# Performance work log

Measured on AMD Instinct MI355X. Metric: run time of the kernel, lower is better.

The kernel has to match this reference:

```python
import jax, jax.numpy as jnp
import numpy as np

N_INPUTS = 128
N_LATENT = 21
LEN_TIME = 51
NUM_SHIFTS = 50
BATCH = 2048
N_HIDDEN = 4  # hidden relu layers in the outer DenseResBlock


def setup_inputs() -> dict:
    key = jax.random.key(0)
    ks = jax.random.split(key, 8)
    s = 0.05  # small init scale keeps activations sane through the residual stack
    return {
        "inputs": jax.random.normal(ks[0], (BATCH, LEN_TIME, N_INPUTS), jnp.float32),
        "L": jnp.eye(N_LATENT, dtype=jnp.float32)
             + s * jax.random.normal(ks[1], (N_LATENT, N_LATENT), jnp.float32),
        "ienc_W": s * jax.random.normal(ks[2], (N_INPUTS, N_LATENT), jnp.float32),
        "idec_W": s * jax.random.normal(ks[3], (N_LATENT, N_INPUTS), jnp.float32),
        "enc_W": s * jax.random.normal(ks[4], (N_HIDDEN, N_INPUTS, N_INPUTS), jnp.float32),
        "enc_b": jnp.zeros((N_HIDDEN, N_INPUTS), jnp.float32),
        "enc_Wo": s * jax.random.normal(ks[5], (N_INPUTS, N_INPUTS), jnp.float32),
        "enc_bo": jnp.zeros((N_INPUTS,), jnp.float32),
        "dec_W": s * jax.random.normal(ks[6], (N_HIDDEN, N_INPUTS, N_INPUTS), jnp.float32),
        "dec_b": jnp.zeros((N_HIDDEN, N_INPUTS), jnp.float32),
        "dec_Wo": s * jax.random.normal(ks[7], (N_INPUTS, N_INPUTS), jnp.float32),
        "dec_bo": jnp.zeros((N_INPUTS,), jnp.float32),
    }


def _resblock(x, W, b, Wo, bo):
    # DenseResBlock: stack of relu Dense layers + linear output + residual skip.
    h = x
    for i in range(W.shape[0]):  # fixed small layer count
        h = jax.nn.relu(h @ W[i] + b[i])
    return x + h @ Wo + bo


def reference(inputs, L, ienc_W, idec_W, enc_W, enc_b, enc_Wo, enc_bo,
              dec_W, dec_b, dec_Wo, dec_bo):
    B, T, n_in = inputs.shape
    len_pred = T - NUM_SHIFTS  # = 1

    auto_in = inputs.reshape(-1, n_in)                        # [B*T, n_in]
    pred_in = inputs[:, :len_pred, :].reshape(-1, n_in)       # [B*len_pred, n_in]

    # autoencoder path
    pe = _resblock(auto_in, enc_W, enc_b, enc_Wo, enc_bo)     # partially encoded
    fe = pe @ ienc_W                                          # fully encoded [., n_latent]
    pd = fe @ idec_W                                          # partially decoded
    autoencoder_output = _resblock(pd, dec_W, dec_b, dec_Wo, dec_bo)
    outer_auto_output = _resblock(pe, dec_W, dec_b, dec_Wo, dec_bo)

    # latent rollout: z_{k+1} = z_k @ L, decode every step
    pe_pred = _resblock(pred_in, enc_W, enc_b, enc_Wo, enc_bo)
    z0 = pe_pred @ ienc_W                                     # [B*len_pred, n_latent]

    def step(z, _):
        z_next = z @ L
        return z_next, z_next

    _, zs = jax.lax.scan(step, z0, None, length=NUM_SHIFTS)   # [S, B*len_pred, n_latent]

    # decode all shifts in one large batched pass (same math as per-shift decode)
    dec_in = zs.reshape(-1, zs.shape[-1]) @ idec_W            # [S*B*len_pred, n_in]
    dec_all = _resblock(dec_in, dec_W, dec_b, dec_Wo, dec_bo)
    predictions = (dec_all
                   .reshape(NUM_SHIFTS, B, len_pred, n_in)
                   .transpose(1, 0, 2, 3)
                   .reshape(B, NUM_SHIFTS * len_pred, n_in))

    return autoencoder_output, outer_auto_output, predictions
```

## Files before the change

### kernel.cpp

```cpp
#include <hip/hip_runtime.h>

#define NF 128
#define NLAT 21
#define NBATCH 2048
#define LEN_T 51
#define NSHIFT 50
#define AUTO_ROWS (NBATCH*LEN_T)
#define PRED_ROWS (NBATCH*NSHIFT)

typedef short bh8  __attribute__((ext_vector_type(8)));
typedef short bh4  __attribute__((ext_vector_type(4)));
typedef unsigned short us8 __attribute__((ext_vector_type(8)));
typedef float f32x4  __attribute__((ext_vector_type(4)));
typedef float f32x16 __attribute__((ext_vector_type(16)));
typedef unsigned u32x4 __attribute__((ext_vector_type(4)));

#define MFMA32(A,B,C) __builtin_amdgcn_mfma_f32_32x32x16_bf16(A,B,C,0,0,0)
#define SGB(m,n) __builtin_amdgcn_sched_group_barrier((m),(n),0)

__device__ __forceinline__ float bf2f(short s){
  unsigned u = ((unsigned)(unsigned short)s) << 16;
  return __builtin_bit_cast(float, u);
}
__device__ __forceinline__ short f2bf(float v){
  unsigned u = __builtin_bit_cast(unsigned, v);
  return (short)((u + 0x7FFFu + ((u>>16)&1u)) >> 16);
}
__device__ __forceinline__ unsigned pk2(float a, float b){
  unsigned ua = __builtin_bit_cast(unsigned, a) + 0x8000u;
  unsigned ub = __builtin_bit_cast(unsigned, b) + 0x8000u;
  return (ua >> 16) | (ub & 0xFFFF0000u);
}

__global__ void k_mmul(const float* __restrict__ ienc, const float* __restrict__ idec,
                       float* __restrict__ M){
  int idx = blockIdx.x*256 + threadIdx.x;
  int i = idx>>7, j = idx&127;
  float s = 0.f;
#pragma unroll
  for(int k=0;k<NLAT;++k) s = fmaf(ienc[i*NLAT+k], idec[k*NF+j], s);
  M[idx] = s;
}

__global__ void k_prep(const float* __restrict__ encW, const float* __restrict__ encWo,
                       const float* __restrict__ decW, const float* __restrict__ decWo,
                       const float* __restrict__ M,    const float* __restrict__ idec,
                       unsigned short* __restrict__ swz){
  int id  = blockIdx.x*256 + threadIdx.x;
  int mat = id >> 11;
  int rem = id & 2047;
  int f   = rem >> 6, l = rem & 63;
  int s   = f >> 2,  mt = f & 3;
  int hl  = l >> 5,  c  = l & 31;
  const float* src;
  if(mat<4)       src = encW + mat*16384;
  else if(mat==4) src = encWo;
  else if(mat<9)  src = decW + (mat-5)*16384;
  else if(mat==9) src = decWo;
  else if(mat==10)src = M;
  else            src = idec;
  us8 w8;
#pragma unroll
  for(int i=0;i<8;++i){
    int k = s*16 + 4*hl + (i&3) + 8*(i>>2);
    float v;
    if(mat==11) v = (k<NLAT) ? src[k*NF + mt*32 + c] : 0.f;
    else        v = src[k*NF + mt*32 + c];
    w8[i] = (unsigned short)f2bf(v);
  }
  *(us8*)(swz + (size_t)mat*16384 + (size_t)f*512 + (size_t)l*8) = w8;
}

__device__ __forceinline__ void stage_issue(const unsigned short* g,
                                            unsigned short* lds, int wid, int lane){
  const unsigned short* gp = g + wid*512 + lane*8;
  unsigned short* lp = lds + wid*512;
#pragma unroll
  for(int i=0;i<8;++i){
    __builtin_amdgcn_global_load_lds(
      (const __attribute__((address_space(1))) void*)(gp + i*2048),
      (__attribute__((address_space(3))) void*)(lp + i*2048), 16, 0, 0);
  }
}

__device__ __forceinline__ void run_half(const unsigned short* wl, int m,
    const bh8 h[16], f32x16 acc[4], int lane){
  f32x16 z;
#pragma unroll
  for(int r=0;r<16;++r) z[r]=0.f;
  acc[0]=z; acc[1]=z; acc[2]=z; acc[3]=z;
  const unsigned short* base = wl + m*1024 + lane*8;
  bh8 a0 = *(const bh8*)(base);
  bh8 a1 = *(const bh8*)(base + 512);
#pragma unroll
  for(int s=0;s<8;++s){
    bh8 b0, b1;
    if(s<7){
      b0 = *(const bh8*)(base + (s+1)*2048);
      b1 = *(const bh8*)(base + (s+1)*2048 + 512);
      SGB(0x100,2);
    }
    __builtin_amdgcn_s_setprio(1);
    acc[0]=MFMA32(a0,h[s],  acc[0]);
    acc[1]=MFMA32(a1,h[s],  acc[1]);
    acc[2]=MFMA32(a0,h[8+s],acc[2]);
    acc[3]=MFMA32(a1,h[8+s],acc[3]);
    __builtin_amdgcn_s_setprio(0);
    SGB(0x8,4);
    if(s<7){ a0=b0; a1=b1; }
  }
}

__device__ __forceinline__ void run_half_k2(const unsigned short* wl, int m,
    const bh8 zf[4], f32x16 acc[4], int lane){
  f32x16 z;
#pragma unroll
  for(int r=0;r<16;++r) z[r]=0.f;
  acc[0]=z; acc[1]=z; acc[2]=z; acc[3]=z;
  const unsigned short* base = wl + m*1024 + lane*8;
#pragma unroll
  for(int s=0;s<2;++s){
    bh8 a0 = *(const bh8*)(base + s*2048);
    bh8 a1 = *(const bh8*)(base + s*2048 + 512);
    acc[0]=MFMA32(a0,zf[s],  acc[0]);
    acc[1]=MFMA32(a1,zf[s],  acc[1]);
    acc[2]=MFMA32(a0,zf[2+s],acc[2]);
    acc[3]=MFMA32(a1,zf[2+s],acc[3]);
  }
}

__device__ __forceinline__ void epi_hidden_half(const f32x16 acc[4], const float* bl,
    int m, int hl, bh8 out[8]){
#pragma unroll
  for(int t=0;t<2;++t){
    f32x4 b[4];
#pragma unroll
    for(int q=0;q<4;++q) b[q] = *(const f32x4*)(bl + (2*m+t)*32 + q*8 + hl*4);
#pragma unroll
    for(int g=0;g<2;++g){
      f32x16 a = acc[g*2+t];
#pragma unroll
      for(int q=0;q<4;++q)
#pragma unroll
        for(int j=0;j<4;++j) a[q*4+j] = fmaxf(a[q*4+j] + b[q][j], 0.f);
#pragma unroll
      for(int p=0;p<2;++p){
        u32x4 w;
#pragma unroll
        for(int j=0;j<4;++j) w[j] = pk2(a[p*8+2*j], a[p*8+2*j+1]);
        out[g*4+t*2+p] = __builtin_bit_cast(bh8, w);
      }
    }
  }
}
__device__ __forceinline__ void epi_plain_half(const f32x16 acc[4], bh8 out[8]){
#pragma unroll
  for(int t=0;t<2;++t)
#pragma unroll
    for(int g=0;g<2;++g){
      f32x16 a = acc[g*2+t];
#pragma unroll
      for(int p=0;p<2;++p){
        u32x4 w;
#pragma unroll
        for(int j=0;j<4;++j) w[j] = pk2(a[p*8+2*j], a[p*8+2*j+1]);
        out[g*4+t*2+p] = __builtin_bit_cast(bh8, w);
      }
    }
}

__device__ __forceinline__ void final_half(float* outp, size_t ro0, size_t ro1,
    const f32x16 acc[4], const float* bo, const bh8 res[16], int m, int hl){
#pragma unroll
  for(int t=0;t<2;++t){
    f32x4 b[4];
#pragma unroll
    for(int q=0;q<4;++q) b[q]=*(const f32x4*)(bo + (2*m+t)*32 + q*8 + hl*4);
#pragma unroll
    for(int g=0;g<2;++g){
      f32x16 a = acc[g*2+t];
      bh8 r0 = res[g*8+(2*m+t)*2], r1 = res[g*8+(2*m+t)*2+1];
#pragma unroll
      for(int q=0;q<4;++q)
#pragma unroll
        for(int j=0;j<4;++j){
          int r=q*4+j;
          a[r] += b[q][j] + bf2f((r<8 ? r0 : r1)[r&7]);
        }
      size_t ro = g ? ro1 : ro0;
#pragma unroll
      for(int q=0;q<4;++q){
        f32x4 w; w[0]=a[q*4+0]; w[1]=a[q*4+1]; w[2]=a[q*4+2]; w[3]=a[q*4+3];
        *(f32x4*)(outp + ro + (2*m+t)*32 + q*8 + hl*4) = w;
      }
    }
  }
}

__device__ __forceinline__ void peWo_half(const f32x16 acc[4], const float* bo,
    const bh8 res[16], int m, int hl, bh8 out[8], float* __restrict__ pe0,
    int bidx0, int bidx1, bool isz0, bool isz1){
#pragma unroll
  for(int t=0;t<2;++t){
    f32x4 b[4];
#pragma unroll
    for(int q=0;q<4;++q) b[q]=*(const f32x4*)(bo + (2*m+t)*32 + q*8 + hl*4);
#pragma unroll
    for(int g=0;g<2;++g){
      f32x16 a = acc[g*2+t];
      bh8 r0 = res[g*8+(2*m+t)*2], r1 = res[g*8+(2*m+t)*2+1];
#pragma unroll
      for(int q=0;q<4;++q)
#pragma unroll
        for(int j=0;j<4;++j){
          int r=q*4+j;
          a[r] += b[q][j] + bf2f((r<8 ? r0 : r1)[r&7]);
        }
      bool isz = g ? isz1 : isz0;
      int bidx = g ? bidx1 : bidx0;
      if(isz){
#pragma unroll
        for(int q=0;q<4;++q){
          f32x4 w; w[0]=a[q*4+0]; w[1]=a[q*4+1]; w[2]=a[q*4+2]; w[3]=a[q*4+3];
          *(f32x4*)(pe0 + (size_t)bidx*NF + (2*m+t)*32 + q*8 + hl*4) = w;
        }
      }
#pragma unroll
      for(int p=0;p<2;++p){
        u32x4 w;
#pragma unroll
        for(int j=0;j<4;++j) w[j]=pk2(a[p*8+2*j], a[p*8+2*j+1]);
        out[g*4+t*2+p]=__builtin_bit_cast(bh8,w);
      }
    }
  }
}

__device__ __forceinline__ void layer_hidden(const unsigned short* wl, const float* bl,
    bh8 h[16], int lane, int hl){
  f32x16 acc[4]; bh8 t0[8], t1[8];
  run_half(wl,0,h,acc,lane);
  epi_hidden_half(acc,bl,0,hl,t0);
  run_half(wl,1,h,acc,lane);
  epi_hidden_half(acc,bl,1,hl,t1);
#pragma unroll
  for(int g=0;g<2;++g)
#pragma unroll
    for(int k=0;k<4;++k){ h[g*8+k]=t0[g*4+k]; h[g*8+4+k]=t1[g*4+k]; }
}

__device__ __forceinline__ void stash16(unsigned short* sp, const bh8 h[16], int lane){
#pragma unroll
  for(int f=0;f<16;++f) *(bh8*)(sp + f*512 + (size_t)lane*8) = h[f];
}
__device__ __forceinline__ void unstash16(const unsigned short* sp, bh8 r[16], int lane){
#pragma unroll
  for(int f=0;f<16;++f) r[f] = *(const bh8*)(sp + f*512 + (size_t)lane*8);
}
__device__ __forceinline__ void stash_rows(unsigned short* o3, const bh8 h[16],
    int orow0, int orow1, int hl){
#pragma unroll
  for(int g=0;g<2;++g){
    size_t rb = (size_t)(g?orow1:orow0)*256;
#pragma unroll
    for(int s=0;s<8;++s){
      bh8 v=h[g*8+s];
      bh4 lo=__builtin_shufflevector(v,v,0,1,2,3);
      bh4 hi=__builtin_shufflevector(v,v,4,5,6,7);
      *(bh4*)(o3 + rb + s*16 + 4*hl) = lo;
      *(bh4*)(o3 + rb + s*16 + 8 + 4*hl) = hi;
    }
  }
}
__device__ __forceinline__ void unstash_rows(const unsigned short* o3, bh8 r[16],
    int orow0, int orow1, int hl){
#pragma unroll
  for(int g=0;g<2;++g){
    size_t rb=(size_t)(g?orow1:orow0)*256;
#pragma unroll
    for(int s=0;s<8;++s){
      bh4 lo=*(const bh4*)(o3 + rb + s*16 + 4*hl);
      bh4 hi=*(const bh4*)(o3 + rb + s*16 + 8 + 4*hl);
      r[g*8+s]=__builtin_shufflevector(lo,hi,0,1,2,3,4,5,6,7);
    }
  }
}

__global__ __launch_bounds__(256,2)
void k_main3(const float* __restrict__ gin, const unsigned short* __restrict__ swz,
             const float* __restrict__ encB, const float* __restrict__ encBo,
             const float* __restrict__ decB, const float* __restrict__ decBo,
             float* out1, float* out2, float* __restrict__ pe0){
  __shared__ __align__(16) unsigned short wlds[2][16384];
  __shared__ __align__(16) float blds[1280];
  const int tid=threadIdx.x, lane=tid&63, wid=tid>>6;
  const int hl=lane>>5, c31=lane&31;
  const size_t rowbase = (size_t)blockIdx.x*256 + wid*64;
  const int row0 = (int)rowbase + c31, row1 = row0 + 32;
  unsigned short* st2 = (unsigned short*)out2 + rowbase*256;
  unsigned short* st1 = (unsigned short*)out1 + rowbase*256;
  const size_t ro0 = (size_t)row0*NF, ro1 = (size_t)row1*NF;
  const int bidx0 = row0/LEN_T, bidx1 = row1/LEN_T;
  const bool isz0 = (row0 == bidx0*LEN_T), isz1 = (row1 == bidx1*LEN_T);
  bh8 h[16], res[16];

  stage_issue(swz, wlds[0], wid, lane);
  for(int i=tid;i<1280;i+=256)
    blds[i] = (i<512)?encB[i] : (i<1024)?decB[i-512] : (i<1152)?encBo[i-1024] : decBo[i-1152];

#pragma unroll
  for(int g=0;g<2;++g){
    const float* rp = gin + (g?ro1:ro0);
#pragma unroll
    for(int s=0;s<8;++s){
      f32x4 a=*(const f32x4*)(rp + s*16 + 4*hl);
      f32x4 b=*(const f32x4*)(rp + s*16 + 8 + 4*hl);
      us8 o;
#pragma unroll
      for(int i=0;i<4;++i){ o[i]=(unsigned short)f2bf(a[i]); o[i+4]=(unsigned short)f2bf(b[i]); }
      h[g*8+s]=__builtin_bit_cast(bh8,o);
    }
  }
  stash16(st2, h, lane);
  __syncthreads();
  int cur=0;

#pragma unroll 1
  for(int l=0;l<4;++l){
    unsigned short* wc = cur?wlds[1]:wlds[0];
    unsigned short* wn = cur?wlds[0]:wlds[1];
    stage_issue(swz + (size_t)(l+1)*16384, wn, wid, lane);
    layer_hidden(wc, blds + l*NF, h, lane, hl);
    __syncthreads(); cur^=1;
  }
  {
    unstash16(st2, res, lane);
    unsigned short* wc = cur?wlds[1]:wlds[0];
    unsigned short* wn = cur?wlds[0]:wlds[1];
    stage_issue(swz + (size_t)5*16384, wn, wid, lane);
    f32x16 acc[4]; bh8 t0[8], t1[8];
    run_half(wc,0,h,acc,lane);
    peWo_half(acc, blds+1024, res, 0, hl, t0, pe0, bidx0,bidx1, isz0,isz1);
    run_half(wc,1,h,acc,lane);
    peWo_half(acc, blds+1024, res, 1, hl, t1, pe0, bidx0,bidx1, isz0,isz1);
#pragma unroll
    for(int g=0;g<2;++g)
#pragma unroll
      for(int k=0;k<4;++k){ h[g*8+k]=t0[g*4+k]; h[g*8+4+k]=t1[g*4+k]; }
    stash16(st2, h, lane);
    __syncthreads(); cur^=1;
  }
#pragma unroll 1
  for(int l=0;l<4;++l){
    unsigned short* wc = cur?wlds[1]:wlds[0];
    unsigned short* wn = cur?wlds[0]:wlds[1];
    stage_issue(swz + (size_t)(6+l)*16384, wn, wid, lane);
    layer_hidden(wc, blds + 512 + l*NF, h, lane, hl);
    __syncthreads(); cur^=1;
  }
  {
    unstash16(st2, res, lane);
    unsigned short* wc = cur?wlds[1]:wlds[0];
    unsigned short* wn = cur?wlds[0]:wlds[1];
    stage_issue(swz + (size_t)10*16384, wn, wid, lane);
    f32x16 acc[4];
    run_half(wc,0,h,acc,lane);
    final_half(out2, ro0, ro1, acc, blds+1152, res, 0, hl);
    run_half(wc,1,h,acc,lane);
    final_half(out2, ro0, ro1, acc, blds+1152, res, 1, hl);
    __syncthreads(); cur^=1;
  }
  {
    unsigned short* wc = cur?wlds[1]:wlds[0];
    unsigned short* wn = cur?wlds[0]:wlds[1];
    stage_issue(swz + (size_t)5*16384, wn, wid, lane);
    f32x16 acc[4]; bh8 t0[8], t1[8];
    run_half(wc,0,res,acc,lane); epi_plain_half(acc,t0);
    run_half(wc,1,res,acc,lane); epi_plain_half(acc,t1);
#pragma unroll
    for(int g=0;g<2;++g)
#pragma unroll
      for(int k=0;k<4;++k){ h[g*8+k]=t0[g*4+k]; h[g*8+4+k]=t1[g*4+k]; }
    stash16(st1, h, lane);
    __syncthreads(); cur^=1;
  }
#pragma unroll 1
  for(int l=0;l<4;++l){
    unsigned short* wc = cur?wlds[1]:wlds[0];
    unsigned short* wn = cur?wlds[0]:wlds[1];
    stage_issue(swz + (size_t)(6+l)*16384, wn, wid, lane);
    layer_hidden(wc, blds + 512 + l*NF, h, lane, hl);
    __syncthreads(); cur^=1;
  }
  {
    unstash16(st1, res, lane);
    unsigned short* wc = cur?wlds[1]:wlds[0];
    f32x16 acc[4];
    run_half(wc,0,h,acc,lane);
    final_half(out1, ro0, ro1, acc, blds+1152, res, 0, hl);
    run_half(wc,1,h,acc,lane);
    final_half(out1, ro0, ro1, acc, blds+1152, res, 1, hl);
  }
}

__global__ void k_roll(const float* __restrict__ pe0, const float* __restrict__ ienc,
                       const float* __restrict__ L, float* __restrict__ zs){
  const int tid=threadIdx.x, lane=tid&63, wid=tid>>6, sub=lane&31, half=lane>>5;
  const int row=blockIdx.x*8 + wid*2 + half;
  const bool act = sub < NLAT;
  float Lc[NLAT];
#pragma unroll
  for(int k=0;k<NLAT;++k) Lc[k] = act ? L[k*NLAT+sub] : 0.f;
  float z=0.f;
  if(act){
    const float* pr = pe0 + (size_t)row*NF;
    float s0=0.f,s1=0.f,s2=0.f,s3=0.f;
#pragma unroll 8
    for(int k=0;k<NF;k+=4){
      s0=fmaf(pr[k+0], ienc[(k+0)*NLAT+sub], s0);
      s1=fmaf(pr[k+1], ienc[(k+1)*NLAT+sub], s1);
      s2=fmaf(pr[k+2], ienc[(k+2)*NLAT+sub], s2);
      s3=fmaf(pr[k+3], ienc[(k+3)*NLAT+sub], s3);
    }
    z=(s0+s1)+(s2+s3);
  }
  const int base = half*32;
#pragma unroll 1
  for(int s=0;s<NSHIFT;++s){
    float zn=0.f;
#pragma unroll
    for(int k=0;k<NLAT;++k) zn=fmaf(__shfl(z, base+k, 64), Lc[k], zn);
    z=zn;
    if(act) zs[((size_t)s*NBATCH + row)*NLAT + sub] = z;
  }
}

__global__ __launch_bounds__(256,2)
void k_pred3(const float* __restrict__ zs, const unsigned short* __restrict__ swz,
             const float* __restrict__ decB, const float* __restrict__ decBo,
             float* out3){
  __shared__ __align__(16) unsigned short wlds[2][16384];
  __shared__ __align__(16) float blds[640];
  const int tid=threadIdx.x, lane=tid&63, wid=tid>>6;
  const int hl=lane>>5, c31=lane&31;
  const size_t rowbase = (size_t)blockIdx.x*256 + wid*64;
  const int prow0 = (int)rowbase + c31, prow1 = prow0 + 32;
  const int orow0 = (prow0 & 2047)*NSHIFT + (prow0 >> 11);
  const int orow1 = (prow1 & 2047)*NSHIFT + (prow1 >> 11);
  bh8 h[16], res[16];

  stage_issue(swz + (size_t)11*16384, wlds[0], wid, lane);
  for(int i=tid;i<640;i+=256) blds[i] = (i<512) ? decB[i] : decBo[i-512];

  bh8 zf[4];
#pragma unroll
  for(int g=0;g<2;++g){
    const float* zr = zs + (size_t)(g?prow1:prow0)*NLAT;
#pragma unroll
    for(int s=0;s<2;++s){
      us8 o;
#pragma unroll
      for(int i=0;i<8;++i){
        int cc = s*16 + 4*hl + (i&3) + 8*(i>>2);
        o[i] = (cc<NLAT) ? (unsigned short)f2bf(zr[cc]) : (unsigned short)0;
      }
      zf[g*2+s]=__builtin_bit_cast(bh8,o);
    }
  }
  __syncthreads();
  int cur=0;

  {
    unsigned short* wc = wlds[0];
    unsigned short* wn = wlds[1];
    stage_issue(swz + (size_t)5*16384, wn, wid, lane);
    f32x16 acc[4]; bh8 t0[8], t1[8];
    run_half_k2(wc,0,zf,acc,lane); epi_plain_half(acc,t0);
    run_half_k2(wc,1,zf,acc,lane); epi_plain_half(acc,t1);
#pragma unroll
    for(int g=0;g<2;++g)
#pragma unroll
      for(int k=0;k<4;++k){ h[g*8+k]=t0[g*4+k]; h[g*8+4+k]=t1[g*4+k]; }
    stash_rows((unsigned short*)out3, h, orow0, orow1, hl);
    __syncthreads(); cur=1;
  }
#pragma unroll 1
  for(int l=0;l<4;++l){
    unsigned short* wc = cur?wlds[1]:wlds[0];
    unsigned short* wn = cur?wlds[0]:wlds[1];
    stage_issue(swz + (size_t)(6+l)*16384, wn, wid, lane);
    layer_hidden(wc, blds + l*NF, h, lane, hl);
    __syncthreads(); cur^=1;
  }
  {
    unstash_rows((const unsigned short*)out3, res, orow0, orow1, hl);
    unsigned short* wc = cur?wlds[1]:wlds[0];
    f32x16 acc[4];
    run_half(wc,0,h,acc,lane);
    final_half(out3, (size_t)orow0*NF, (size_t)orow1*NF, acc, blds+512, res, 0, hl);
    run_half(wc,1,h,acc,lane);
    final_half(out3, (size_t)orow0*NF, (size_t)orow1*NF, acc, blds+512, res, 1, hl);
  }
}

extern "C" void kernel_launch(void* const* d_in, const int* in_sizes, int n_in,
                              void* d_out, int out_size, void* d_ws, size_t ws_size,
                              hipStream_t stream) {
  const float* gin   = (const float*)d_in[0];
  const float* L     = (const float*)d_in[1];
  const float* iencW = (const float*)d_in[2];
  const float* idecW = (const float*)d_in[3];
  const float* encW  = (const float*)d_in[4];
  const float* encB  = (const float*)d_in[5];
  const float* encWo = (const float*)d_in[6];
  const float* encBo = (const float*)d_in[7];
  const float* decW  = (const float*)d_in[8];
  const float* decB  = (const float*)d_in[9];
  const float* decWo = (const float*)d_in[10];
  const float* decBo = (const float*)d_in[11];

  float* out1 = (float*)d_out;
  float* out2 = out1 + (size_t)AUTO_ROWS*NF;
  float* out3 = out2 + (size_t)AUTO_ROWS*NF;

  float* M   = (float*)d_ws;
  float* pe0 = M + 16384;
  float* zs  = pe0 + (size_t)NBATCH*NF;
  unsigned short* swz = (unsigned short*)(zs + (size_t)NSHIFT*NBATCH*NLAT);

  hipLaunchKernelGGL(k_mmul, dim3(64),  dim3(256), 0, stream, iencW, idecW, M);
  hipLaunchKernelGGL(k_prep, dim3(96),  dim3(256), 0, stream, encW, encWo, decW, decWo, M, idecW, swz);
  hipLaunchKernelGGL(k_main3, dim3(AUTO_ROWS/256), dim3(256), 0, stream,
                     gin, swz, encB, encBo, decB, decBo, out1, out2, pe0);
  hipLaunchKernelGGL(k_roll, dim3(NBATCH/8), dim3(256), 0, stream, pe0, iencW, L, zs);
  hipLaunchKernelGGL(k_pred3, dim3(PRED_ROWS/256), dim3(256), 0, stream,
                     zs, swz, decB, decBo, out3);
}
```

Baseline: 170.4 us.

## Read MFMA weights directly from global/L2 in single-wave blocks instead of LDS staging

Drops the double-buffered LDS weight staging and __syncthreads barriers, and reshapes blocks to a single 64-lane wave. Each wave now reads the pre-swizzled bf16 weight fragments straight from global memory (relying on L1/L2 cache) with a two-step register prefetch. Residual stashes move from scratch space in the output buffers into a small per-block LDS buffer, and biases are read directly from global memory. This removes block-level sync stalls and the LDS copy traffic, at the cost of every wave separately re-reading the weights through the cache hierarchy, with more exposed load latency.

```diff
diff --git a/kernel.cpp b/kernel.cpp
--- a/kernel.cpp
+++ b/kernel.cpp
@@ -9,7 +9,6 @@
 #define PRED_ROWS (NBATCH*NSHIFT)
 
 typedef short bh8  __attribute__((ext_vector_type(8)));
-typedef short bh4  __attribute__((ext_vector_type(4)));
 typedef unsigned short us8 __attribute__((ext_vector_type(8)));
 typedef float f32x4  __attribute__((ext_vector_type(4)));
 typedef float f32x16 __attribute__((ext_vector_type(16)));
@@ -71,57 +70,50 @@
   *(us8*)(swz + (size_t)mat*16384 + (size_t)f*512 + (size_t)l*8) = w8;
 }
 
-__device__ __forceinline__ void stage_issue(const unsigned short* g,
-                                            unsigned short* lds, int wid, int lane){
-  const unsigned short* gp = g + wid*512 + lane*8;
-  unsigned short* lp = lds + wid*512;
-#pragma unroll
-  for(int i=0;i<8;++i){
-    __builtin_amdgcn_global_load_lds(
-      (const __attribute__((address_space(1))) void*)(gp + i*2048),
-      (__attribute__((address_space(3))) void*)(lp + i*2048), 16, 0, 0);
-  }
-}
-
-__device__ __forceinline__ void run_half(const unsigned short* wl, int m,
+__device__ __forceinline__ bh8 ldg8(const unsigned short* p){ return *(const bh8*)p; }
+
+__device__ __forceinline__ void run_half(const unsigned short* __restrict__ wg, int m,
     const bh8 h[16], f32x16 acc[4], int lane){
   f32x16 z;
 #pragma unroll
   for(int r=0;r<16;++r) z[r]=0.f;
   acc[0]=z; acc[1]=z; acc[2]=z; acc[3]=z;
-  const unsigned short* base = wl + m*1024 + lane*8;
-  bh8 a0 = *(const bh8*)(base);
-  bh8 a1 = *(const bh8*)(base + 512);
+  const unsigned short* base = wg + m*1024 + lane*8;
+  bh8 w0a = ldg8(base);
+  bh8 w0b = ldg8(base + 512);
+  bh8 w1a = ldg8(base + 2048);
+  bh8 w1b = ldg8(base + 2048 + 512);
 #pragma unroll
   for(int s=0;s<8;++s){
-    bh8 b0, b1;
-    if(s<7){
-      b0 = *(const bh8*)(base + (s+1)*2048);
-      b1 = *(const bh8*)(base + (s+1)*2048 + 512);
-      SGB(0x100,2);
+    bh8 na, nb;
+    if(s<6){
+      na = ldg8(base + (s+2)*2048);
+      nb = ldg8(base + (s+2)*2048 + 512);
+      SGB(0x20,2);
     }
     __builtin_amdgcn_s_setprio(1);
-    acc[0]=MFMA32(a0,h[s],  acc[0]);
-    acc[1]=MFMA32(a1,h[s],  acc[1]);
-    acc[2]=MFMA32(a0,h[8+s],acc[2]);
-    acc[3]=MFMA32(a1,h[8+s],acc[3]);
+    acc[0]=MFMA32(w0a,h[s],  acc[0]);
+    acc[1]=MFMA32(w0b,h[s],  acc[1]);
+    acc[2]=MFMA32(w0a,h[8+s],acc[2]);
+    acc[3]=MFMA32(w0b,h[8+s],acc[3]);
     __builtin_amdgcn_s_setprio(0);
     SGB(0x8,4);
-    if(s<7){ a0=b0; a1=b1; }
-  }
-}
-
-__device__ __forceinline__ void run_half_k2(const unsigned short* wl, int m,
+    if(s<6){ w0a=w1a; w0b=w1b; w1a=na; w1b=nb; }
+    else    { w0a=w1a; w0b=w1b; }
+  }
+}
+
+__device__ __forceinline__ void run_half_k2(const unsigned short* __restrict__ wg, int m,
     const bh8 zf[4], f32x16 acc[4], int lane){
   f32x16 z;
 #pragma unroll
   for(int r=0;r<16;++r) z[r]=0.f;
   acc[0]=z; acc[1]=z; acc[2]=z; acc[3]=z;
-  const unsigned short* base = wl + m*1024 + lane*8;
+  const unsigned short* base = wg + m*1024 + lane*8;
 #pragma unroll
   for(int s=0;s<2;++s){
-    bh8 a0 = *(const bh8*)(base + s*2048);
-    bh8 a1 = *(const bh8*)(base + s*2048 + 512);
+    bh8 a0 = ldg8(base + s*2048);
+    bh8 a1 = ldg8(base + s*2048 + 512);
     acc[0]=MFMA32(a0,zf[s],  acc[0]);
     acc[1]=MFMA32(a1,zf[s],  acc[1]);
     acc[2]=MFMA32(a0,zf[2+s],acc[2]);
@@ -129,7 +121,7 @@
   }
 }
 
-__device__ __forceinline__ void epi_hidden_half(const f32x16 acc[4], const float* bl,
+__device__ __forceinline__ void epi_hidden_half(const f32x16 acc[4], const float* __restrict__ bl,
     int m, int hl, bh8 out[8]){
 #pragma unroll
   for(int t=0;t<2;++t){
@@ -170,7 +162,7 @@
 }
 
 __device__ __forceinline__ void final_half(float* outp, size_t ro0, size_t ro1,
-    const f32x16 acc[4], const float* bo, const bh8 res[16], int m, int hl){
+    const f32x16 acc[4], const float* __restrict__ bo, const bh8 r8[8], int m, int hl){
 #pragma unroll
   for(int t=0;t<2;++t){
     f32x4 b[4];
@@ -179,7 +171,7 @@
 #pragma unroll
     for(int g=0;g<2;++g){
       f32x16 a = acc[g*2+t];
-      bh8 r0 = res[g*8+(2*m+t)*2], r1 = res[g*8+(2*m+t)*2+1];
+      bh8 r0 = r8[g*4 + t*2], r1 = r8[g*4 + t*2 + 1];
 #pragma unroll
       for(int q=0;q<4;++q)
 #pragma unroll
@@ -197,8 +189,8 @@
   }
 }
 
-__device__ __forceinline__ void peWo_half(const f32x16 acc[4], const float* bo,
-    const bh8 res[16], int m, int hl, bh8 out[8], float* __restrict__ pe0,
+__device__ __forceinline__ void peWo_half(const f32x16 acc[4], const float* __restrict__ bo,
+    const bh8 r8[8], int m, int hl, bh8 out[8], float* __restrict__ pe0,
     int bidx0, int bidx1, bool isz0, bool isz1){
 #pragma unroll
   for(int t=0;t<2;++t){
@@ -208,7 +200,7 @@
 #pragma unroll
     for(int g=0;g<2;++g){
       f32x16 a = acc[g*2+t];
-      bh8 r0 = res[g*8+(2*m+t)*2], r1 = res[g*8+(2*m+t)*2+1];
+      bh8 r0 = r8[g*4 + t*2], r1 = r8[g*4 + t*2 + 1];
 #pragma unroll
       for(int q=0;q<4;++q)
 #pragma unroll
@@ -236,12 +228,12 @@
   }
 }
 
-__device__ __forceinline__ void layer_hidden(const unsigned short* wl, const float* bl,
-    bh8 h[16], int lane, int hl){
+__device__ __forceinline__ void layer_hidden(const unsigned short* __restrict__ wg,
+    const float* __restrict__ bl, bh8 h[16], int lane, int hl){
   f32x16 acc[4]; bh8 t0[8], t1[8];
-  run_half(wl,0,h,acc,lane);
+  run_half(wg,0,h,acc,lane);
   epi_hidden_half(acc,bl,0,hl,t0);
-  run_half(wl,1,h,acc,lane);
+  run_half(wg,1,h,acc,lane);
   epi_hidden_half(acc,bl,1,hl,t1);
 #pragma unroll
   for(int g=0;g<2;++g)
@@ -251,62 +243,34 @@
 
 __device__ __forceinline__ void stash16(unsigned short* sp, const bh8 h[16], int lane){
 #pragma unroll
-  for(int f=0;f<16;++f) *(bh8*)(sp + f*512 + (size_t)lane*8) = h[f];
+  for(int f=0;f<16;++f) *(bh8*)(sp + f*512 + lane*8) = h[f];
 }
 __device__ __forceinline__ void unstash16(const unsigned short* sp, bh8 r[16], int lane){
 #pragma unroll
-  for(int f=0;f<16;++f) r[f] = *(const bh8*)(sp + f*512 + (size_t)lane*8);
-}
-__device__ __forceinline__ void stash_rows(unsigned short* o3, const bh8 h[16],
-    int orow0, int orow1, int hl){
-#pragma unroll
-  for(int g=0;g<2;++g){
-    size_t rb = (size_t)(g?orow1:orow0)*256;
-#pragma unroll
-    for(int s=0;s<8;++s){
-      bh8 v=h[g*8+s];
-      bh4 lo=__builtin_shufflevector(v,v,0,1,2,3);
-      bh4 hi=__builtin_shufflevector(v,v,4,5,6,7);
-      *(bh4*)(o3 + rb + s*16 + 4*hl) = lo;
-      *(bh4*)(o3 + rb + s*16 + 8 + 4*hl) = hi;
-    }
-  }
-}
-__device__ __forceinline__ void unstash_rows(const unsigned short* o3, bh8 r[16],
-    int orow0, int orow1, int hl){
-#pragma unroll
-  for(int g=0;g<2;++g){
-    size_t rb=(size_t)(g?orow1:orow0)*256;
-#pragma unroll
-    for(int s=0;s<8;++s){
-      bh4 lo=*(const bh4*)(o3 + rb + s*16 + 4*hl);
-      bh4 hi=*(const bh4*)(o3 + rb + s*16 + 8 + 4*hl);
-      r[g*8+s]=__builtin_shufflevector(lo,hi,0,1,2,3,4,5,6,7);
-    }
-  }
-}
-
-__global__ __launch_bounds__(256,2)
-void k_main3(const float* __restrict__ gin, const unsigned short* __restrict__ swz,
+  for(int f=0;f<16;++f) r[f] = *(const bh8*)(sp + f*512 + lane*8);
+}
+__device__ __forceinline__ void unstash8(const unsigned short* sp, bh8 r8[8], int m, int lane){
+#pragma unroll
+  for(int g=0;g<2;++g)
+#pragma unroll
+    for(int k=0;k<4;++k)
+      r8[g*4+k] = *(const bh8*)(sp + (g*8 + 4*m + k)*512 + lane*8);
+}
+
+__global__ __launch_bounds__(64,2)
+void k_main4(const float* __restrict__ gin, const unsigned short* __restrict__ swz,
              const float* __restrict__ encB, const float* __restrict__ encBo,
              const float* __restrict__ decB, const float* __restrict__ decBo,
-             float* out1, float* out2, float* __restrict__ pe0){
-  __shared__ __align__(16) unsigned short wlds[2][16384];
-  __shared__ __align__(16) float blds[1280];
-  const int tid=threadIdx.x, lane=tid&63, wid=tid>>6;
-  const int hl=lane>>5, c31=lane&31;
-  const size_t rowbase = (size_t)blockIdx.x*256 + wid*64;
+             float* __restrict__ out1, float* __restrict__ out2, float* __restrict__ pe0){
+  __shared__ __align__(16) unsigned short sres[8192];
+  const int lane = threadIdx.x;
+  const int hl = lane>>5, c31 = lane&31;
+  const size_t rowbase = (size_t)blockIdx.x*64;
   const int row0 = (int)rowbase + c31, row1 = row0 + 32;
-  unsigned short* st2 = (unsigned short*)out2 + rowbase*256;
-  unsigned short* st1 = (unsigned short*)out1 + rowbase*256;
   const size_t ro0 = (size_t)row0*NF, ro1 = (size_t)row1*NF;
   const int bidx0 = row0/LEN_T, bidx1 = row1/LEN_T;
   const bool isz0 = (row0 == bidx0*LEN_T), isz1 = (row1 == bidx1*LEN_T);
-  bh8 h[16], res[16];
-
-  stage_issue(swz, wlds[0], wid, lane);
-  for(int i=tid;i<1280;i+=256)
-    blds[i] = (i<512)?encB[i] : (i<1024)?decB[i-512] : (i<1152)?encBo[i-1024] : decBo[i-1152];
+  bh8 h[16];
 
 #pragma unroll
   for(int g=0;g<2;++g){
@@ -321,85 +285,69 @@
       h[g*8+s]=__builtin_bit_cast(bh8,o);
     }
   }
-  stash16(st2, h, lane);
-  __syncthreads();
-  int cur=0;
+  stash16(sres, h, lane);
 
 #pragma unroll 1
-  for(int l=0;l<4;++l){
-    unsigned short* wc = cur?wlds[1]:wlds[0];
-    unsigned short* wn = cur?wlds[0]:wlds[1];
-    stage_issue(swz + (size_t)(l+1)*16384, wn, wid, lane);
-    layer_hidden(wc, blds + l*NF, h, lane, hl);
-    __syncthreads(); cur^=1;
-  }
-  {
-    unstash16(st2, res, lane);
-    unsigned short* wc = cur?wlds[1]:wlds[0];
-    unsigned short* wn = cur?wlds[0]:wlds[1];
-    stage_issue(swz + (size_t)5*16384, wn, wid, lane);
+  for(int l=0;l<4;++l)
+    layer_hidden(swz + (size_t)l*16384, encB + l*NF, h, lane, hl);
+
+  {
+    const unsigned short* wg = swz + (size_t)4*16384;
+    f32x16 acc[4]; bh8 t0[8], t1[8], r8[8];
+    run_half(wg,0,h,acc,lane);
+    unstash8(sres, r8, 0, lane);
+    peWo_half(acc, encBo, r8, 0, hl, t0, pe0, bidx0,bidx1, isz0,isz1);
+    run_half(wg,1,h,acc,lane);
+    unstash8(sres, r8, 1, lane);
+    peWo_half(acc, encBo, r8, 1, hl, t1, pe0, bidx0,bidx1, isz0,isz1);
+#pragma unroll
+    for(int g=0;g<2;++g)
+#pragma unroll
+      for(int k=0;k<4;++k){ h[g*8+k]=t0[g*4+k]; h[g*8+4+k]=t1[g*4+k]; }
+    stash16(sres, h, lane);
+  }
+
+#pragma unroll 1
+  for(int l=0;l<4;++l)
+    layer_hidden(swz + (size_t)(5+l)*16384, decB + l*NF, h, lane, hl);
+
+  {
+    const unsigned short* wg = swz + (size_t)9*16384;
+    f32x16 acc[4]; bh8 r8[8];
+    run_half(wg,0,h,acc,lane);
+    unstash8(sres, r8, 0, lane);
+    final_half(out2, ro0, ro1, acc, decBo, r8, 0, hl);
+    run_half(wg,1,h,acc,lane);
+    unstash8(sres, r8, 1, lane);
+    final_half(out2, ro0, ro1, acc, decBo, r8, 1, hl);
+  }
+
+  {
+    unstash16(sres, h, lane);
+    const unsigned short* wg = swz + (size_t)10*16384;
     f32x16 acc[4]; bh8 t0[8], t1[8];
-    run_half(wc,0,h,acc,lane);
-    peWo_half(acc, blds+1024, res, 0, hl, t0, pe0, bidx0,bidx1, isz0,isz1);
-    run_half(wc,1,h,acc,lane);
-    peWo_half(acc, blds+1024, res, 1, hl, t1, pe0, bidx0,bidx1, isz0,isz1);
+    run_half(wg,0,h,acc,lane); epi_plain_half(acc,t0);
+    run_half(wg,1,h,acc,lane); epi_plain_half(acc,t1);
 #pragma unroll
     for(int g=0;g<2;++g)
 #pragma unroll
       for(int k=0;k<4;++k){ h[g*8+k]=t0[g*4+k]; h[g*8+4+k]=t1[g*4+k]; }
-    stash16(st2, h, lane);
-    __syncthreads(); cur^=1;
-  }
+    stash16(sres, h, lane);
+  }
+
 #pragma unroll 1
-  for(int l=0;l<4;++l){
-    unsigned short* wc = cur?wlds[1]:wlds[0];
-    unsigned short* wn = cur?wlds[0]:wlds[1];
-    stage_issue(swz + (size_t)(6+l)*16384, wn, wid, lane);
-    layer_hidden(wc, blds + 512 + l*NF, h, lane, hl);
-    __syncthreads(); cur^=1;
-  }
-  {
-    unstash16(st2, res, lane);
-    unsigned short* wc = cur?wlds[1]:wlds[0];
-    unsigned short* wn = cur?wlds[0]:wlds[1];
-    stage_issue(swz + (size_t)10*16384, wn, wid, lane);
-    f32x16 acc[4];
-    run_half(wc,0,h,acc,lane);
-    final_half(out2, ro0, ro1, acc, blds+1152, res, 0, hl);
-    run_half(wc,1,h,acc,lane);
-    final_half(out2, ro0, ro1, acc, blds+1152, res, 1, hl);
-    __syncthreads(); cur^=1;
-  }
-  {
-    unsigned short* wc = cur?wlds[1]:wlds[0];
-    unsigned short* wn = cur?wlds[0]:wlds[1];
-    stage_issue(swz + (size_t)5*16384, wn, wid, lane);
-    f32x16 acc[4]; bh8 t0[8], t1[8];
-    run_half(wc,0,res,acc,lane); epi_plain_half(acc,t0);
-    run_half(wc,1,res,acc,lane); epi_plain_half(acc,t1);
-#pragma unroll
-    for(int g=0;g<2;++g)
-#pragma unroll
-      for(int k=0;k<4;++k){ h[g*8+k]=t0[g*4+k]; h[g*8+4+k]=t1[g*4+k]; }
-    stash16(st1, h, lane);
-    __syncthreads(); cur^=1;
-  }
-#pragma unroll 1
-  for(int l=0;l<4;++l){
-    unsigned short* wc = cur?wlds[1]:wlds[0];
-    unsigned short* wn = cur?wlds[0]:wlds[1];
-    stage_issue(swz + (size_t)(6+l)*16384, wn, wid, lane);
-    layer_hidden(wc, blds + 512 + l*NF, h, lane, hl);
-    __syncthreads(); cur^=1;
-  }
-  {
-    unstash16(st1, res, lane);
-    unsigned short* wc = cur?wlds[1]:wlds[0];
-    f32x16 acc[4];
-    run_half(wc,0,h,acc,lane);
-    final_half(out1, ro0, ro1, acc, blds+1152, res, 0, hl);
-    run_half(wc,1,h,acc,lane);
-    final_half(out1, ro0, ro1, acc, blds+1152, res, 1, hl);
+  for(int l=0;l<4;++l)
+    layer_hidden(swz + (size_t)(5+l)*16384, decB + l*NF, h, lane, hl);
+
+  {
+    const unsigned short* wg = swz + (size_t)9*16384;
+    f32x16 acc[4]; bh8 r8[8];
+    run_half(wg,0,h,acc,lane);
+    unstash8(sres, r8, 0, lane);
+    final_half(out1, ro0, ro1, acc, decBo, r8, 0, hl);
+    run_half(wg,1,h,acc,lane);
+    unstash8(sres, r8, 1, lane);
+    final_half(out1, ro0, ro1, acc, decBo, r8, 1, hl);
   }
 }
 
@@ -435,22 +383,18 @@
   }
 }
 
-__global__ __launch_bounds__(256,2)
-void k_pred3(const float* __restrict__ zs, const unsigned short* __restrict__ swz,
+__global__ __launch_bounds__(64,2)
+void k_pred4(const float* __restrict__ zs, const unsigned short* __restrict__ swz,
              const float* __restrict__ decB, const float* __restrict__ decBo,
-             float* out3){
-  __shared__ __align__(16) unsigned short wlds[2][16384];
-  __shared__ __align__(16) float blds[640];
-  const int tid=threadIdx.x, lane=tid&63, wid=tid>>6;
-  const int hl=lane>>5, c31=lane&31;
-  const size_t rowbase = (size_t)blockIdx.x*256 + wid*64;
+             float* __restrict__ out3){
+  __shared__ __align__(16) unsigned short sres[8192];
+  const int lane = threadIdx.x;
+  const int hl = lane>>5, c31 = lane&31;
+  const size_t rowbase = (size_t)blockIdx.x*64;
   const int prow0 = (int)rowbase + c31, prow1 = prow0 + 32;
   const int orow0 = (prow0 & 2047)*NSHIFT + (prow0 >> 11);
   const int orow1 = (prow1 & 2047)*NSHIFT + (prow1 >> 11);
-  bh8 h[16], res[16];
-
-  stage_issue(swz + (size_t)11*16384, wlds[0], wid, lane);
-  for(int i=tid;i<640;i+=256) blds[i] = (i<512) ? decB[i] : decBo[i-512];
+  bh8 h[16];
 
   bh8 zf[4];
 #pragma unroll
@@ -467,39 +411,32 @@
       zf[g*2+s]=__builtin_bit_cast(bh8,o);
     }
   }
-  __syncthreads();
-  int cur=0;
-
-  {
-    unsigned short* wc = wlds[0];
-    unsigned short* wn = wlds[1];
-    stage_issue(swz + (size_t)5*16384, wn, wid, lane);
+
+  {
+    const unsigned short* wg = swz + (size_t)11*16384;
     f32x16 acc[4]; bh8 t0[8], t1[8];
-    run_half_k2(wc,0,zf,acc,lane); epi_plain_half(acc,t0);
-    run_half_k2(wc,1,zf,acc,lane); epi_plain_half(acc,t1);
+    run_half_k2(wg,0,zf,acc,lane); epi_plain_half(acc,t0);
+    run_half_k2(wg,1,zf,acc,lane); epi_plain_half(acc,t1);
 #pragma unroll
     for(int g=0;g<2;++g)
 #pragma unroll
       for(int k=0;k<4;++k){ h[g*8+k]=t0[g*4+k]; h[g*8+4+k]=t1[g*4+k]; }
-    stash_rows((unsigned short*)out3, h, orow0, orow1, hl);
-    __syncthreads(); cur=1;
-  }
+    stash16(sres, h, lane);
+  }
+
 #pragma unroll 1
-  for(int l=0;l<4;++l){
-    unsigned short* wc = cur?wlds[1]:wlds[0];
-    unsigned short* wn = cur?wlds[0]:wlds[1];
-    stage_issue(swz + (size_t)(6+l)*16384, wn, wid, lane);
-    layer_hidden(wc, blds + l*NF, h, lane, hl);
-    __syncthreads(); cur^=1;
-  }
-  {
-    unstash_rows((const unsigned short*)out3, res, orow0, orow1, hl);
-    unsigned short* wc = cur?wlds[1]:wlds[0];
-    f32x16 acc[4];
-    run_half(wc,0,h,acc,lane);
-    final_half(out3, (size_t)orow0*NF, (size_t)orow1*NF, acc, blds+512, res, 0, hl);
-    run_half(wc,1,h,acc,lane);
-    final_half(out3, (size_t)orow0*NF, (size_t)orow1*NF, acc, blds+512, res, 1, hl);
+  for(int l=0;l<4;++l)
+    layer_hidden(swz + (size_t)(5+l)*16384, decB + l*NF, h, lane, hl);
+
+  {
+    const unsigned short* wg = swz + (size_t)9*16384;
+    f32x16 acc[4]; bh8 r8[8];
+    run_half(wg,0,h,acc,lane);
+    unstash8(sres, r8, 0, lane);
+    final_half(out3, (size_t)orow0*NF, (size_t)orow1*NF, acc, decBo, r8, 0, hl);
+    run_half(wg,1,h,acc,lane);
+    unstash8(sres, r8, 1, lane);
+    final_half(out3, (size_t)orow0*NF, (size_t)orow1*NF, acc, decBo, r8, 1, hl);
   }
 }
 
@@ -530,9 +467,9 @@
 
   hipLaunchKernelGGL(k_mmul, dim3(64),  dim3(256), 0, stream, iencW, idecW, M);
   hipLaunchKernelGGL(k_prep, dim3(96),  dim3(256), 0, stream, encW, encWo, decW, decWo, M, idecW, swz);
-  hipLaunchKernelGGL(k_main3, dim3(AUTO_ROWS/256), dim3(256), 0, stream,
+  hipLaunchKernelGGL(k_main4, dim3(AUTO_ROWS/64), dim3(64), 0, stream,
                      gin, swz, encB, encBo, decB, decBo, out1, out2, pe0);
   hipLaunchKernelGGL(k_roll, dim3(NBATCH/8), dim3(256), 0, stream, pe0, iencW, L, zs);
-  hipLaunchKernelGGL(k_pred3, dim3(PRED_ROWS/256), dim3(256), 0, stream,
+  hipLaunchKernelGGL(k_pred4, dim3(PRED_ROWS/64), dim3(64), 0, stream,
                      zs, swz, decB, decBo, out3);
 }
```

After: 153.2 us. 1.11x faster.
